# Kernel tuning notes

Measured on AMD Instinct MI355X. Metric: run time of the kernel, lower is better.

The kernel has to match this reference:

```python
import jax, jax.numpy as jnp
import numpy as np

N_NODES = 50000
N_EDGES = 800000
D_FEAT = 256
HIDDEN = 256
N_CLASSES = 10
N_GRAPHS = 128


def setup_inputs() -> dict:
    key = jax.random.key(0)
    ks = jax.random.split(key, 16)
    x = jax.random.normal(ks[0], (N_NODES, D_FEAT), dtype=jnp.float32)
    edge_index = jax.random.randint(ks[1], (2, N_EDGES), 0, N_NODES, dtype=jnp.int64)
    batch = jnp.sort(jax.random.randint(ks[2], (N_NODES,), 0, N_GRAPHS, dtype=jnp.int64))
    def lin(k, fin, fout):
        s = 1.0 / np.sqrt(fin)
        return jax.random.uniform(k, (fin, fout), jnp.float32, -s, s)
    return {
        "x": x, "edge_index": edge_index, "batch": batch,
        "W0": lin(ks[3], D_FEAT, HIDDEN), "b0": jnp.zeros((HIDDEN,), jnp.float32),
        "W1": lin(ks[4], HIDDEN, HIDDEN), "b1": jnp.zeros((HIDDEN,), jnp.float32),
        "W2": lin(ks[5], HIDDEN, HIDDEN), "b2": jnp.zeros((HIDDEN,), jnp.float32),
        "fc1_W": lin(ks[6], HIDDEN, HIDDEN), "fc1_b": jnp.zeros((HIDDEN,), jnp.float32),
        "fc2_W": lin(ks[7], HIDDEN, N_CLASSES), "fc2_b": jnp.zeros((N_CLASSES,), jnp.float32),
    }


def _gcn_norm(edge_index, n_nodes):
    # PyG GCNConv: add self-loops, deg from (A+I) with unit weights,
    # norm_e = deg^{-1/2}[src] * deg^{-1/2}[dst]
    loop = jnp.arange(n_nodes, dtype=edge_index.dtype)
    src = jnp.concatenate([edge_index[0], loop])
    dst = jnp.concatenate([edge_index[1], loop])
    deg = jax.ops.segment_sum(jnp.ones_like(dst, dtype=jnp.float32), dst,
                              num_segments=n_nodes)
    dinv = jnp.where(deg > 0, jax.lax.rsqrt(deg), 0.0)
    norm = dinv[src] * dinv[dst]
    return src, dst, norm


def _gcn_conv(x, src, dst, norm, W, b, n_nodes):
    h = x @ W                              # [N, out]
    msg = h[src] * norm[:, None]           # gather + scale  [E+N, out]
    out = jax.ops.segment_sum(msg, dst, num_segments=n_nodes)  # scatter-add
    return out + b


def reference(x, edge_index, batch, W0, b0, W1, b1, W2, b2, fc1_W, fc1_b, fc2_W, fc2_b):
    n_nodes = x.shape[0]
    src, dst, norm = _gcn_norm(edge_index, n_nodes)
    h = jax.nn.relu(_gcn_conv(x, src, dst, norm, W0, b0, n_nodes))
    h = jax.nn.relu(_gcn_conv(h, src, dst, norm, W1, b1, n_nodes))
    h = jax.nn.relu(_gcn_conv(h, src, dst, norm, W2, b2, n_nodes))
    # global add pool over graphs
    g = jax.ops.segment_sum(h, batch, num_segments=N_GRAPHS)   # [G, H]
    g = jax.nn.relu(g @ fc1_W + fc1_b)
    # dropout p=0.5 is identity in eval mode
    logits = g @ fc2_W + fc2_b
    return jax.nn.log_softmax(logits, axis=-1)
```

## Files before the change

### kernel.cpp

```cpp
#include <hip/hip_runtime.h>
#include <math.h>

#define FDIM 256
#define NGRAPH 128
#define NCLASS 10

typedef short short8 __attribute__((ext_vector_type(8)));
typedef float floatx4 __attribute__((ext_vector_type(4)));

static __device__ __forceinline__ unsigned short f2bf(float f) {
    unsigned u = __float_as_uint(f);
    u += 0x7FFF + ((u >> 16) & 1);
    return (unsigned short)(u >> 16);
}
static __device__ __forceinline__ float bflo(unsigned u) { return __uint_as_float(u << 16); }
static __device__ __forceinline__ float bfhi(unsigned u) { return __uint_as_float(u & 0xFFFF0000u); }


__global__ __launch_bounds__(256) void prep_kernel(const int* __restrict__ dst,
                                                   int* __restrict__ cnt,
                                                   unsigned short* __restrict__ slot,
                                                   int E, int nCnt,
                                                   const float* __restrict__ W0,
                                                   const float* __restrict__ W1,
                                                   const float* __restrict__ W2,
                                                   unsigned short* __restrict__ Bp0,
                                                   unsigned short* __restrict__ Bp1,
                                                   unsigned short* __restrict__ Bp2,
                                                   float4* __restrict__ g4) {
    const int b = blockIdx.x;
    const int t = threadIdx.x;
    if (b < nCnt) {
        int e = b * 256 + t;
        if (e < E) slot[e] = (unsigned short)atomicAdd(&cnt[dst[e]], 1);
        return;
    }
    const int b2 = b - nCnt;
    if (b2 >= 96) {
        g4[(size_t)(b2 - 96) * 256 + t] = (float4){0.f, 0.f, 0.f, 0.f};
        return;
    }
    const float* W = (b2 < 32) ? W0 : (b2 < 64) ? W1 : W2;
    unsigned short* Bp = (b2 < 32) ? Bp0 : (b2 < 64) ? Bp1 : Bp2;
    int idx = (b2 & 31) * 256 + t;
    int kstep = idx >> 10;
    int ntile = (idx >> 6) & 15;
    int lane  = idx & 63;
    int col   = ntile * 16 + (lane & 15);
    int krow  = kstep * 32 + (lane >> 4) * 8;
    unsigned short o[8];
#pragma unroll
    for (int j = 0; j < 8; j++) o[j] = f2bf(W[(size_t)(krow + j) * FDIM + col]);
    *(uint4*)(Bp + (size_t)idx * 8) = *(uint4*)o;
}


__global__ __launch_bounds__(256) void csr_bsum(const int* __restrict__ cnt,
                                                int* __restrict__ bsum, int N) {
    __shared__ int red[256];
    const int t = threadIdx.x;
    const int base = blockIdx.x * 1024 + t * 4;
    int s = 0;
#pragma unroll
    for (int i = 0; i < 4; i++)
        if (base + i < N) s += (cnt[base + i] + 7) & ~7;
    red[t] = s;
    __syncthreads();
    for (int off = 128; off > 0; off >>= 1) {
        if (t < off) red[t] += red[t + off];
        __syncthreads();
    }
    if (t == 0) bsum[blockIdx.x] = red[0];
}

__global__ __launch_bounds__(256) void csr_scan2(const int* __restrict__ cnt,
                                                 const int* __restrict__ bsum,
                                                 int* __restrict__ rowptr,
                                                 float* __restrict__ dinv, int N) {
    __shared__ int redo[256];
    __shared__ int tsum[256];
    const int t = threadIdx.x;
    const int bid = blockIdx.x;

    int pre = 0;
    for (int i = t; i < bid; i += 256) pre += bsum[i];
    redo[t] = pre;
    __syncthreads();
    for (int off = 128; off > 0; off >>= 1) {
        if (t < off) redo[t] += redo[t + off];
        __syncthreads();
    }
    const int blockoff = redo[0];
    __syncthreads();

    const int base = bid * 1024 + t * 4;
    int c[4], pc[4];
    int s = 0;
#pragma unroll
    for (int i = 0; i < 4; i++) {
        c[i] = (base + i < N) ? cnt[base + i] : 0;
        pc[i] = (c[i] + 7) & ~7;
        s += pc[i];
    }
    tsum[t] = s;
    __syncthreads();
    for (int off = 1; off < 256; off <<= 1) {
        int v = (t >= off) ? tsum[t - off] : 0;
        __syncthreads();
        tsum[t] += v;
        __syncthreads();
    }
    int run = blockoff + ((t == 0) ? 0 : tsum[t - 1]);
#pragma unroll
    for (int i = 0; i < 4; i++) {
        int idx = base + i;
        if (idx < N) {
            rowptr[idx] = run;
            dinv[idx] = rsqrtf((float)c[i] + 1.0f);
            run += pc[i];
            if (idx == N - 1) rowptr[N] = run;
        }
    }
}


template<int AFP32>
static __device__ __forceinline__ void gemm_tile64(const void* __restrict__ A,
                                                   const unsigned short* __restrict__ Bp,
                                                   unsigned short* __restrict__ C,
                                                   int M, int tile) {
    const int wave = threadIdx.x >> 6;
    const int lane = threadIdx.x & 63;
    const int quad = lane >> 4;
    const int m    = lane & 15;
    const int row0 = tile * 64;

    short8 breg[8][4];
#pragma unroll
    for (int ks = 0; ks < 8; ks++)
#pragma unroll
        for (int j = 0; j < 4; j++)
            breg[ks][j] = *(const short8*)((const short*)Bp +
                            ((size_t)((ks * 16 + wave * 4 + j) * 64 + lane) * 8));

#pragma unroll
    for (int mt = 0; mt < 4; mt++) {
        const int r0 = min(row0 + mt * 16 + m, M - 1);
        floatx4 acc[4];
#pragma unroll
        for (int j = 0; j < 4; j++) acc[j] = (floatx4){0.f, 0.f, 0.f, 0.f};
#pragma unroll
        for (int ks = 0; ks < 8; ks++) {
            short8 a;
            if (AFP32) {
                const float* ar = (const float*)A + (size_t)r0 * FDIM + ks * 32 + quad * 8;
                float4 p0 = *(const float4*)ar;
                float4 p1 = *(const float4*)(ar + 4);
                a[0] = (short)f2bf(p0.x); a[1] = (short)f2bf(p0.y);
                a[2] = (short)f2bf(p0.z); a[3] = (short)f2bf(p0.w);
                a[4] = (short)f2bf(p1.x); a[5] = (short)f2bf(p1.y);
                a[6] = (short)f2bf(p1.z); a[7] = (short)f2bf(p1.w);
            } else {
                a = *(const short8*)((const short*)A + (size_t)r0 * FDIM + ks * 32 + quad * 8);
            }
#pragma unroll
            for (int j = 0; j < 4; j++)
                acc[j] = __builtin_amdgcn_mfma_f32_16x16x32_bf16(a, breg[ks][j], acc[j], 0, 0, 0);
        }
#pragma unroll
        for (int j = 0; j < 4; j++) {
            int col = (wave * 4 + j) * 16 + m;
#pragma unroll
            for (int r = 0; r < 4; r++) {
                int row = row0 + mt * 16 + quad * 4 + r;
                if (row < M) C[(size_t)row * FDIM + col] = f2bf(acc[j][r]);
            }
        }
    }
}

__global__ __launch_bounds__(256, 2) void gemm0_fill_kernel(const float* __restrict__ x,
                                                            const unsigned short* __restrict__ Bp0,
                                                            unsigned short* __restrict__ H,
                                                            int M, int ng,
                                                            const int* __restrict__ src,
                                                            const int* __restrict__ dst,
                                                            const int* __restrict__ rowptr,
                                                            const unsigned short* __restrict__ slot,
                                                            unsigned short* __restrict__ srcs,
                                                            float* __restrict__ normv,
                                                            const float* __restrict__ dinv, int E) {
    if ((int)blockIdx.x < ng) {
        gemm_tile64<1>(x, Bp0, H, M, blockIdx.x);
        return;
    }
    int e = (blockIdx.x - ng) * 256 + threadIdx.x;
    if (e < E) {
        int s = src[e], d = dst[e];
        int r = rowptr[d] + (int)slot[e];
        srcs[r] = (unsigned short)s;
        normv[r] = dinv[s] * dinv[d];
    }
}

__global__ __launch_bounds__(256, 2) void mfma_gemm(const unsigned short* __restrict__ A,
                                                    const unsigned short* __restrict__ Bp,
                                                    unsigned short* __restrict__ C, int M) {
    gemm_tile64<0>(A, Bp, C, M, blockIdx.x);
}


static __device__ __forceinline__ void gather_node64(const unsigned short* __restrict__ h,
                                                     const int* __restrict__ rowptr,
                                                     const unsigned short* __restrict__ srcs,
                                                     const float* __restrict__ normv,
                                                     const float* __restrict__ dinv,
                                                     const float* __restrict__ bias,
                                                     int node, int lane, float* acc) {
    const float di = dinv[node];
    const float dii = di * di;
    uint2 sv = *(const uint2*)(h + (size_t)node * FDIM + lane * 4);
    float4 b = *(const float4*)(bias + lane * 4);
    acc[0] = dii * bflo(sv.x) + b.x;
    acc[1] = dii * bfhi(sv.x) + b.y;
    acc[2] = dii * bflo(sv.y) + b.z;
    acc[3] = dii * bfhi(sv.y) + b.w;

    const int beg = rowptr[node];
    const int end = rowptr[node + 1];
    for (int p = beg; p < end; p += 8) {
        uint4 s8 = *(const uint4*)(srcs + p);
        float4 n0 = *(const float4*)(normv + p);
        float4 n1 = *(const float4*)(normv + p + 4);
        const unsigned short* sp = (const unsigned short*)&s8;
        uint2 v[8];
#pragma unroll
        for (int i = 0; i < 8; i++)
            v[i] = *(const uint2*)(h + (size_t)sp[i] * FDIM + lane * 4);
        float nm[8] = {n0.x, n0.y, n0.z, n0.w, n1.x, n1.y, n1.z, n1.w};
#pragma unroll
        for (int i = 0; i < 8; i++) {
            acc[0] += nm[i] * bflo(v[i].x);
            acc[1] += nm[i] * bfhi(v[i].x);
            acc[2] += nm[i] * bflo(v[i].y);
            acc[3] += nm[i] * bfhi(v[i].y);
        }
    }
#pragma unroll
    for (int i = 0; i < 4; i++) acc[i] = fmaxf(acc[i], 0.0f);
}

__global__ __launch_bounds__(256) void gather_kernel(const unsigned short* __restrict__ h,
                                                     const int* __restrict__ rowptr,
                                                     const unsigned short* __restrict__ srcs,
                                                     const float* __restrict__ normv,
                                                     const float* __restrict__ dinv,
                                                     const float* __restrict__ bias,
                                                     unsigned short* __restrict__ out, int N) {
    int node = blockIdx.x * 4 + (threadIdx.x >> 6);
    node = __builtin_amdgcn_readfirstlane(node);
    const int lane = threadIdx.x & 63;
    if (node >= N) return;
    float acc[4];
    gather_node64(h, rowptr, srcs, normv, dinv, bias, node, lane, acc);
    unsigned short o[4];
#pragma unroll
    for (int i = 0; i < 4; i++) o[i] = f2bf(acc[i]);
    *(uint2*)(out + (size_t)node * FDIM + lane * 4) = *(uint2*)o;
}

__global__ __launch_bounds__(256) void gather_pool_kernel(const unsigned short* __restrict__ h,
                                                          const int* __restrict__ rowptr,
                                                          const unsigned short* __restrict__ srcs,
                                                          const float* __restrict__ normv,
                                                          const float* __restrict__ dinv,
                                                          const float* __restrict__ bias,
                                                          const int* __restrict__ batch,
                                                          float* __restrict__ g, int N) {
    __shared__ float red[4][FDIM];
    __shared__ int bid[4];
    const int hw   = threadIdx.x >> 6;
    const int lane = threadIdx.x & 63;
    int node = blockIdx.x * 4 + hw;
    node = __builtin_amdgcn_readfirstlane(node);

    float acc[4] = {0.f, 0.f, 0.f, 0.f};
    if (node < N) gather_node64(h, rowptr, srcs, normv, dinv, bias, node, lane, acc);
#pragma unroll
    for (int i = 0; i < 4; i++) red[hw][lane * 4 + i] = acc[i];
    if (lane == 0) bid[hw] = (node < N) ? batch[node] : -1;
    __syncthreads();

    const int f = threadIdx.x;
    int cur = -1;
    float run = 0.0f;
    for (int i = 0; i < 4; i++) {
        int b = bid[i];
        if (b < 0) break;
        if (b != cur) {
            if (cur >= 0) atomicAdd(&g[(size_t)cur * FDIM + f], run);
            cur = b;
            run = 0.0f;
        }
        run += red[i][f];
    }
    if (cur >= 0) atomicAdd(&g[(size_t)cur * FDIM + f], run);
}


__global__ __launch_bounds__(256) void fc_head_kernel(const float* __restrict__ g,
                                                      const float* __restrict__ fc1W,
                                                      const float* __restrict__ fc1b,
                                                      const float* __restrict__ fc2W,
                                                      const float* __restrict__ fc2b,
                                                      float* __restrict__ out) {
    __shared__ float gs[FDIM];
    __shared__ float part[4][FDIM];
    __shared__ float hs[FDIM];
    __shared__ float p2[256];
    __shared__ float logits[NCLASS];
    const int r = blockIdx.x;
    const int t = threadIdx.x;
    const int w = t >> 6;
    const int l = t & 63;

    gs[t] = g[(size_t)r * FDIM + t];
    __syncthreads();

    float a[4] = {0.f, 0.f, 0.f, 0.f};
    for (int kk = 0; kk < 64; kk++) {
        int k = w * 64 + kk;
        float gv = gs[k];
#pragma unroll
        for (int j = 0; j < 4; j++) a[j] += gv * fc1W[(size_t)k * FDIM + j * 64 + l];
    }
#pragma unroll
    for (int j = 0; j < 4; j++) part[w][j * 64 + l] = a[j];
    __syncthreads();

    float s1 = part[0][t] + part[1][t] + part[2][t] + part[3][t] + fc1b[t];
    hs[t] = fmaxf(s1, 0.0f);
    __syncthreads();

    float a2 = 0.0f;
    const int c = t & 15;
    if (c < NCLASS) {
        int k0 = (t >> 4) * 16;
        for (int kk = 0; kk < 16; kk++)
            a2 += hs[k0 + kk] * fc2W[(size_t)(k0 + kk) * NCLASS + c];
    }
    p2[t] = a2;
    __syncthreads();

    if (t < NCLASS) {
        float s2 = fc2b[t];
        for (int seg = 0; seg < 16; seg++) s2 += p2[seg * 16 + t];
        logits[t] = s2;
    }
    __syncthreads();

    if (t == 0) {
        float mx = logits[0];
        for (int cc = 1; cc < NCLASS; cc++) mx = fmaxf(mx, logits[cc]);
        float ssum = 0.0f;
        for (int cc = 0; cc < NCLASS; cc++) ssum += expf(logits[cc] - mx);
        float lse = mx + logf(ssum);
        for (int cc = 0; cc < NCLASS; cc++) out[(size_t)r * NCLASS + cc] = logits[cc] - lse;
    }
}


extern "C" void kernel_launch(void* const* d_in, const int* in_sizes, int n_in,
                              void* d_out, int out_size, void* d_ws, size_t ws_size,
                              hipStream_t stream) {
    const float* x     = (const float*)d_in[0];
    const int*   ei    = (const int*)d_in[1];
    const int*   batch = (const int*)d_in[2];
    const float* W0 = (const float*)d_in[3];  const float* b0 = (const float*)d_in[4];
    const float* W1 = (const float*)d_in[5];  const float* b1 = (const float*)d_in[6];
    const float* W2 = (const float*)d_in[7];  const float* b2 = (const float*)d_in[8];
    const float* fc1W = (const float*)d_in[9];  const float* fc1b = (const float*)d_in[10];
    const float* fc2W = (const float*)d_in[11]; const float* fc2b = (const float*)d_in[12];
    float* out = (float*)d_out;

    const int N = in_sizes[0] / FDIM;
    const int E = in_sizes[1] / 2;
    const int* src = ei;
    const int* dst = ei + E;
    const int Mpad = ((N + 63) / 64) * 64;
    const int nb   = (N + 1023) / 1024;
    const int nCnt = (E + 255) / 256;
    const int ng   = (N + 63) / 64;
    const size_t Epad = (size_t)E + 8 * (size_t)N;

    char* p = (char*)d_ws;
    unsigned short* S  = (unsigned short*)p; p += (size_t)Mpad * FDIM * 2;
    unsigned short* H  = (unsigned short*)p; p += (size_t)Mpad * FDIM * 2;
    unsigned short* Wp0 = (unsigned short*)p; p += (size_t)8192 * 8 * 2;
    unsigned short* Wp1 = (unsigned short*)p; p += (size_t)8192 * 8 * 2;
    unsigned short* Wp2 = (unsigned short*)p; p += (size_t)8192 * 8 * 2;
    float* dinv = (float*)p; p += (size_t)N * 4;
    int*   cnt  = (int*)p;   p += (size_t)N * 4;
    int*   rowptr = (int*)p; p += (size_t)(N + 4) * 4;
    int*   bsum = (int*)p;   p += (size_t)256 * 4;
    unsigned short* srcs = (unsigned short*)p; p += ((Epad * 2 + 15) & ~15ull);
    unsigned short* slot = (unsigned short*)p; p += (((size_t)E * 2 + 15) & ~15ull);
    float* normv = (float*)p; p += ((Epad * 4 + 15) & ~15ull);
    float* g    = (float*)p;

    hipMemsetAsync(cnt, 0, (size_t)N * sizeof(int), stream);
    hipMemsetAsync(srcs, 0, Epad * 2, stream);
    hipMemsetAsync(normv, 0, Epad * 4, stream);
    prep_kernel<<<nCnt + 128, 256, 0, stream>>>(dst, cnt, slot, E, nCnt,
                                                W0, W1, W2, Wp0, Wp1, Wp2, (float4*)g);
    csr_bsum<<<nb, 256, 0, stream>>>(cnt, bsum, N);
    csr_scan2<<<nb, 256, 0, stream>>>(cnt, bsum, rowptr, dinv, N);

    gemm0_fill_kernel<<<ng + nCnt, 256, 0, stream>>>(x, Wp0, H, N, ng,
                                                     src, dst, rowptr, slot, srcs, normv, dinv, E);

    gather_kernel<<<(N + 3) / 4, 256, 0, stream>>>(H, rowptr, srcs, normv, dinv, b0, S, N);
    mfma_gemm<<<ng, 256, 0, stream>>>(S, Wp1, H, N);
    gather_kernel<<<(N + 3) / 4, 256, 0, stream>>>(H, rowptr, srcs, normv, dinv, b1, S, N);
    mfma_gemm<<<ng, 256, 0, stream>>>(S, Wp2, H, N);
    gather_pool_kernel<<<(N + 3) / 4, 256, 0, stream>>>(H, rowptr, srcs, normv, dinv, b2,
                                                        batch, g, N);
    fc_head_kernel<<<NGRAPH, 256, 0, stream>>>(g, fc1W, fc1b, fc2W, fc2b, out);
}
```

Baseline: 436.8 us.

## Drop per-edge norm array; compute norm from dinv with sentinel padding row

Removes the normv array and its memset. Each edge weight is now computed inside the gather as dinv[src]*dinv[dst], so there is no longer a stream of 4-byte norms to read per edge. CSR padding slots now point to a sentinel node N, which has a zeroed H/S row and dinv[N]=0, replacing the full memset of srcs. In exchange there is an extra dinv load per neighbor, issued as a scalar load after readfirstlane, plus per-node padding loops in the scan kernel.

```diff
diff --git a/kernel.cpp b/kernel.cpp
--- a/kernel.cpp
+++ b/kernel.cpp
@@ -20,14 +20,16 @@
 __global__ __launch_bounds__(256) void prep_kernel(const int* __restrict__ dst,
                                                    int* __restrict__ cnt,
                                                    unsigned short* __restrict__ slot,
-                                                   int E, int nCnt,
+                                                   int E, int nCnt, int N,
                                                    const float* __restrict__ W0,
                                                    const float* __restrict__ W1,
                                                    const float* __restrict__ W2,
                                                    unsigned short* __restrict__ Bp0,
                                                    unsigned short* __restrict__ Bp1,
                                                    unsigned short* __restrict__ Bp2,
-                                                   float4* __restrict__ g4) {
+                                                   float4* __restrict__ g4,
+                                                   unsigned short* __restrict__ Hrow,
+                                                   unsigned short* __restrict__ Srow) {
     const int b = blockIdx.x;
     const int t = threadIdx.x;
     if (b < nCnt) {
@@ -36,6 +38,11 @@
         return;
     }
     const int b2 = b - nCnt;
+    if (b2 >= 128) {
+        Hrow[(size_t)N * FDIM + t] = 0;
+        Srow[(size_t)N * FDIM + t] = 0;
+        return;
+    }
     if (b2 >= 96) {
         g4[(size_t)(b2 - 96) * 256 + t] = (float4){0.f, 0.f, 0.f, 0.f};
         return;
@@ -76,7 +83,8 @@
 __global__ __launch_bounds__(256) void csr_scan2(const int* __restrict__ cnt,
                                                  const int* __restrict__ bsum,
                                                  int* __restrict__ rowptr,
-                                                 float* __restrict__ dinv, int N) {
+                                                 float* __restrict__ dinv,
+                                                 unsigned short* __restrict__ srcs, int N) {
     __shared__ int redo[256];
     __shared__ int tsum[256];
     const int t = threadIdx.x;
@@ -111,16 +119,19 @@
         __syncthreads();
     }
     int run = blockoff + ((t == 0) ? 0 : tsum[t - 1]);
+    const unsigned short sent = (unsigned short)N;
 #pragma unroll
     for (int i = 0; i < 4; i++) {
         int idx = base + i;
         if (idx < N) {
             rowptr[idx] = run;
             dinv[idx] = rsqrtf((float)c[i] + 1.0f);
+            for (int j = c[i]; j < pc[i]; j++) srcs[run + j] = sent;
             run += pc[i];
             if (idx == N - 1) rowptr[N] = run;
         }
     }
+    if (bid == 0 && t == 0) dinv[N] = 0.0f;
 }
 
 
@@ -187,20 +198,13 @@
                                                             const int* __restrict__ dst,
                                                             const int* __restrict__ rowptr,
                                                             const unsigned short* __restrict__ slot,
-                                                            unsigned short* __restrict__ srcs,
-                                                            float* __restrict__ normv,
-                                                            const float* __restrict__ dinv, int E) {
+                                                            unsigned short* __restrict__ srcs, int E) {
     if ((int)blockIdx.x < ng) {
         gemm_tile64<1>(x, Bp0, H, M, blockIdx.x);
         return;
     }
     int e = (blockIdx.x - ng) * 256 + threadIdx.x;
-    if (e < E) {
-        int s = src[e], d = dst[e];
-        int r = rowptr[d] + (int)slot[e];
-        srcs[r] = (unsigned short)s;
-        normv[r] = dinv[s] * dinv[d];
-    }
+    if (e < E) srcs[rowptr[dst[e]] + (int)slot[e]] = (unsigned short)src[e];
 }
 
 __global__ __launch_bounds__(256, 2) void mfma_gemm(const unsigned short* __restrict__ A,
@@ -213,7 +217,6 @@
 static __device__ __forceinline__ void gather_node64(const unsigned short* __restrict__ h,
                                                      const int* __restrict__ rowptr,
                                                      const unsigned short* __restrict__ srcs,
-                                                     const float* __restrict__ normv,
                                                      const float* __restrict__ dinv,
                                                      const float* __restrict__ bias,
                                                      int node, int lane, float* acc) {
@@ -230,20 +233,23 @@
     const int end = rowptr[node + 1];
     for (int p = beg; p < end; p += 8) {
         uint4 s8 = *(const uint4*)(srcs + p);
-        float4 n0 = *(const float4*)(normv + p);
-        float4 n1 = *(const float4*)(normv + p + 4);
         const unsigned short* sp = (const unsigned short*)&s8;
+        int si[8];
+        float ds[8];
         uint2 v[8];
 #pragma unroll
-        for (int i = 0; i < 8; i++)
-            v[i] = *(const uint2*)(h + (size_t)sp[i] * FDIM + lane * 4);
-        float nm[8] = {n0.x, n0.y, n0.z, n0.w, n1.x, n1.y, n1.z, n1.w};
-#pragma unroll
         for (int i = 0; i < 8; i++) {
-            acc[0] += nm[i] * bflo(v[i].x);
-            acc[1] += nm[i] * bfhi(v[i].x);
-            acc[2] += nm[i] * bflo(v[i].y);
-            acc[3] += nm[i] * bfhi(v[i].y);
+            si[i] = __builtin_amdgcn_readfirstlane((int)sp[i]);
+            ds[i] = dinv[si[i]];
+            v[i] = *(const uint2*)(h + (size_t)si[i] * FDIM + lane * 4);
+        }
+#pragma unroll
+        for (int i = 0; i < 8; i++) {
+            float nm = ds[i] * di;
+            acc[0] += nm * bflo(v[i].x);
+            acc[1] += nm * bfhi(v[i].x);
+            acc[2] += nm * bflo(v[i].y);
+            acc[3] += nm * bfhi(v[i].y);
         }
     }
 #pragma unroll
@@ -253,7 +259,6 @@
 __global__ __launch_bounds__(256) void gather_kernel(const unsigned short* __restrict__ h,
                                                      const int* __restrict__ rowptr,
                                                      const unsigned short* __restrict__ srcs,
-                                                     const float* __restrict__ normv,
                                                      const float* __restrict__ dinv,
                                                      const float* __restrict__ bias,
                                                      unsigned short* __restrict__ out, int N) {
@@ -262,7 +267,7 @@
     const int lane = threadIdx.x & 63;
     if (node >= N) return;
     float acc[4];
-    gather_node64(h, rowptr, srcs, normv, dinv, bias, node, lane, acc);
+    gather_node64(h, rowptr, srcs, dinv, bias, node, lane, acc);
     unsigned short o[4];
 #pragma unroll
     for (int i = 0; i < 4; i++) o[i] = f2bf(acc[i]);
@@ -272,7 +277,6 @@
 __global__ __launch_bounds__(256) void gather_pool_kernel(const unsigned short* __restrict__ h,
                                                           const int* __restrict__ rowptr,
                                                           const unsigned short* __restrict__ srcs,
-                                                          const float* __restrict__ normv,
                                                           const float* __restrict__ dinv,
                                                           const float* __restrict__ bias,
                                                           const int* __restrict__ batch,
@@ -285,7 +289,7 @@
     node = __builtin_amdgcn_readfirstlane(node);
 
     float acc[4] = {0.f, 0.f, 0.f, 0.f};
-    if (node < N) gather_node64(h, rowptr, srcs, normv, dinv, bias, node, lane, acc);
+    if (node < N) gather_node64(h, rowptr, srcs, dinv, bias, node, lane, acc);
 #pragma unroll
     for (int i = 0; i < 4; i++) red[hw][lane * 4 + i] = acc[i];
     if (lane == 0) bid[hw] = (node < N) ? batch[node] : -1;
@@ -394,36 +398,33 @@
     const size_t Epad = (size_t)E + 8 * (size_t)N;
 
     char* p = (char*)d_ws;
-    unsigned short* S  = (unsigned short*)p; p += (size_t)Mpad * FDIM * 2;
-    unsigned short* H  = (unsigned short*)p; p += (size_t)Mpad * FDIM * 2;
+    unsigned short* S  = (unsigned short*)p; p += (size_t)(Mpad + 64) * FDIM * 2;
+    unsigned short* H  = (unsigned short*)p; p += (size_t)(Mpad + 64) * FDIM * 2;
     unsigned short* Wp0 = (unsigned short*)p; p += (size_t)8192 * 8 * 2;
     unsigned short* Wp1 = (unsigned short*)p; p += (size_t)8192 * 8 * 2;
     unsigned short* Wp2 = (unsigned short*)p; p += (size_t)8192 * 8 * 2;
-    float* dinv = (float*)p; p += (size_t)N * 4;
+    float* dinv = (float*)p; p += (((size_t)(N + 1) * 4 + 15) & ~15ull);
     int*   cnt  = (int*)p;   p += (size_t)N * 4;
     int*   rowptr = (int*)p; p += (size_t)(N + 4) * 4;
     int*   bsum = (int*)p;   p += (size_t)256 * 4;
     unsigned short* srcs = (unsigned short*)p; p += ((Epad * 2 + 15) & ~15ull);
     unsigned short* slot = (unsigned short*)p; p += (((size_t)E * 2 + 15) & ~15ull);
-    float* normv = (float*)p; p += ((Epad * 4 + 15) & ~15ull);
     float* g    = (float*)p;
 
     hipMemsetAsync(cnt, 0, (size_t)N * sizeof(int), stream);
-    hipMemsetAsync(srcs, 0, Epad * 2, stream);
-    hipMemsetAsync(normv, 0, Epad * 4, stream);
-    prep_kernel<<<nCnt + 128, 256, 0, stream>>>(dst, cnt, slot, E, nCnt,
-                                                W0, W1, W2, Wp0, Wp1, Wp2, (float4*)g);
+    prep_kernel<<<nCnt + 129, 256, 0, stream>>>(dst, cnt, slot, E, nCnt, N,
+                                                W0, W1, W2, Wp0, Wp1, Wp2, (float4*)g, H, S);
     csr_bsum<<<nb, 256, 0, stream>>>(cnt, bsum, N);
-    csr_scan2<<<nb, 256, 0, stream>>>(cnt, bsum, rowptr, dinv, N);
+    csr_scan2<<<nb, 256, 0, stream>>>(cnt, bsum, rowptr, dinv, srcs, N);
 
     gemm0_fill_kernel<<<ng + nCnt, 256, 0, stream>>>(x, Wp0, H, N, ng,
-                                                     src, dst, rowptr, slot, srcs, normv, dinv, E);
-
-    gather_kernel<<<(N + 3) / 4, 256, 0, stream>>>(H, rowptr, srcs, normv, dinv, b0, S, N);
+                                                     src, dst, rowptr, slot, srcs, E);
+
+    gather_kernel<<<(N + 3) / 4, 256, 0, stream>>>(H, rowptr, srcs, dinv, b0, S, N);
     mfma_gemm<<<ng, 256, 0, stream>>>(S, Wp1, H, N);
-    gather_kernel<<<(N + 3) / 4, 256, 0, stream>>>(H, rowptr, srcs, normv, dinv, b1, S, N);
+    gather_kernel<<<(N + 3) / 4, 256, 0, stream>>>(H, rowptr, srcs, dinv, b1, S, N);
     mfma_gemm<<<ng, 256, 0, stream>>>(S, Wp2, H, N);
-    gather_pool_kernel<<<(N + 3) / 4, 256, 0, stream>>>(H, rowptr, srcs, normv, dinv, b2,
+    gather_pool_kernel<<<(N + 3) / 4, 256, 0, stream>>>(H, rowptr, srcs, dinv, b2,
                                                         batch, g, N);
     fc_head_kernel<<<NGRAPH, 256, 0, stream>>>(g, fc1W, fc1b, fc2W, fc2b, out);
 }
```

Measured after the change: 415.8 us. 4.8% less time.
